# Kernel tuning notes

Hardware: AMD Instinct MI355X
Metric: run time of the kernel (lower is better)

## Reference

```python
import jax, jax.numpy as jnp
import numpy as np

B, DM, DR, DE, E, H, EPS = 4096, 1024, 2048, 1024, 8, 8, 1e-5
SCALE = (DE // H) ** -0.5


def setup_inputs() -> dict:
    key = jax.random.key(0)
    ks = jax.random.split(key, 24)
    n = lambda k, s, sc=0.02: jax.random.normal(k, s, jnp.float32) * sc
    return {
        "x": n(ks[0], (B, DM), 1.0),
        "Wm_mu": n(ks[1], (E, DM, DE)), "bm_mu": jnp.zeros((E, DE)),
        "g_mu": jnp.ones((E, DE)), "be_mu": jnp.zeros((E, DE)),
        "rm_mu": jnp.zeros((E, DE)), "rv_mu": jnp.ones((E, DE)),
        "Wm_d": n(ks[2], (E, DM, DE)), "bm_d": jnp.zeros((E, DE)),
        "g_d": jnp.ones((E, DE)), "be_d": jnp.zeros((E, DE)),
        "rm_d": jnp.zeros((E, DE)), "rv_d": jnp.ones((E, DE)),
        "gw1_mu": n(ks[3], (DM, 64)), "gb1_mu": jnp.zeros((64,)),
        "gw2_mu": n(ks[4], (64, E)), "gb2_mu": jnp.zeros((E,)),
        "gw1_d": n(ks[5], (DM, 64)), "gb1_d": jnp.zeros((64,)),
        "gw2_d": n(ks[6], (64, E)), "gb2_d": jnp.zeros((E,)),
        "Wq": n(ks[7], (DE, DE)), "Wk": n(ks[8], (DE, DE)), "Wv": n(ks[9], (DE, DE)),
        "Wp": n(ks[10], (DE, DE)), "bp": jnp.zeros((DE,)),
        "se_w1": n(ks[11], (DE, DE // 64)), "se_w2": n(ks[12], (DE // 64, DE)),
        "Wr_dec": n(ks[13], (DE, DR)), "br_dec": jnp.zeros((DR,)),
        "gr": jnp.ones((DR,)), "betar": jnp.zeros((DR,)),
        "rmr": jnp.zeros((DR,)), "rvr": jnp.ones((DR,)),
        "Wm_dec": n(ks[14], (DE, DM)), "bm_dec": jnp.zeros((DM,)),
        "gm": jnp.ones((DM,)), "betam": jnp.zeros((DM,)),
        "rmm": jnp.zeros((DM,)), "rvm": jnp.ones((DM,)),
    }


def _bn(h, g, b, rm, rv):  # eval-mode BatchNorm1d
    return (h - rm) * jax.lax.rsqrt(rv + EPS) * g + b


def _moe(x, W, bias, g, be, rm, rv, gw1, gb1, gw2, gb2, act):
    # all-expert Linear+BN+act, gated softmax mixture
    h = jnp.einsum('bd,edh->beh', x, W) + bias            # [B,E,DE]
    h = act(_bn(h, g, be, rm, rv))
    gate = jax.nn.softmax(jax.nn.relu(x @ gw1 + gb1) @ gw2 + gb2, axis=-1)  # [B,E]
    return jnp.einsum('beh,be->bh', h, gate)


def _attn(x, Wq, Wk, Wv, Wp, bp):  # x: [B,N,C], self-attention (context = x)
    b, n, c = x.shape
    hd = c // H
    q = (x @ Wq).reshape(b, n, H, hd).transpose(0, 2, 1, 3)
    k = (x @ Wk).reshape(b, n, H, hd).transpose(0, 2, 1, 3)
    v = (x @ Wv).reshape(b, n, H, hd).transpose(0, 2, 1, 3)
    a = jax.nn.softmax(jnp.einsum('bhnd,bhmd->bhnm', q, k) * SCALE, axis=-1)
    o = jnp.einsum('bhnm,bhmd->bhnd', a, v).transpose(0, 2, 1, 3).reshape(b, n, c)
    return o @ Wp + bp


def reference(x, Wm_mu, bm_mu, g_mu, be_mu, rm_mu, rv_mu,
              Wm_d, bm_d, g_d, be_d, rm_d, rv_d,
              gw1_mu, gb1_mu, gw2_mu, gb2_mu, gw1_d, gb1_d, gw2_d, gb2_d,
              Wq, Wk, Wv, Wp, bp, se_w1, se_w2,
              Wr_dec, br_dec, gr, betar, rmr, rvr,
              Wm_dec, bm_dec, gm, betam, rmm, rvm):
    # Translator.test_model(x, 'MET') == forward_with_MET(x, 'test')
    mu = _moe(x, Wm_mu, bm_mu, g_mu, be_mu, rm_mu, rv_mu,
              gw1_mu, gb1_mu, gw2_mu, gb2_mu, jax.nn.relu)
    d = _moe(x, Wm_d, bm_d, g_d, be_d, rm_d, rv_d,
             gw1_d, gb1_d, gw2_d, gb2_d, jax.nn.relu)
    attn_out = _attn(x[:, None, :], Wq, Wk, Wv, Wp, bp)[:, 0, :]
    mu = mu + attn_out
    latent = mu  # forward_type == 'test'
    # SE layer
    latent = latent * jax.nn.sigmoid(jax.nn.relu(latent @ se_w1) @ se_w2)
    r_out = jax.nn.sigmoid(_bn(latent @ Wr_dec + br_dec, gr, betar, rmr, rvr))
    m_out = jax.nn.sigmoid(_bn(latent @ Wm_dec + bm_dec, gm, betam, rmm, rvm))
    return (r_out, m_out, mu, d)
```

## Files before the change

kernel.cpp:

```cpp
#include <hip/hip_runtime.h>
#include <hip/hip_bf16.h>

typedef __hip_bfloat16 bf16;
typedef __attribute__((ext_vector_type(4))) float f32x4;
typedef __attribute__((ext_vector_type(8))) short s16x8;
typedef __attribute__((ext_vector_type(4))) short s16x4;

#define AS1 __attribute__((address_space(1)))
#define AS3 __attribute__((address_space(3)))

#define NB      4096
#define EPSV    1e-5f

#define OUT_R_OFF   0ull
#define OUT_M_OFF   8388608ull
#define OUT_MU_OFF  12582912ull
#define OUT_D_OFF   16777216ull

__device__ __forceinline__ short f2bf(float f) {
  union { bf16 b; short s; } u;
  u.b = __float2bfloat16(f);
  return u.s;
}
__device__ __forceinline__ float bf2f(short s) {
  union { float f; unsigned u; } v;
  v.u = ((unsigned)(unsigned short)s) << 16;
  return v.f;
}

__device__ __forceinline__ void gl_lds16(const bf16* g, void* l) {
  __builtin_amdgcn_global_load_lds((const AS1 unsigned int*)g,
                                   (AS3 unsigned int*)l, 16, 0, 0);
}

__device__ __forceinline__ void stage_tile_ld1024(const bf16* __restrict__ base,
                                                  int row0, int k0,
                                                  unsigned char* ldsTile,
                                                  int wave, int lane) {
  const int srow = lane >> 3;
  const int gch  = ((lane & 7) + srow) & 7;
  const bf16* g0 = base + ((size_t)(row0 + srow) << 10) + k0 + (gch << 3);
#pragma unroll
  for (int i = 0; i < 4; ++i) {
    const int q = wave * 4 + i;
    gl_lds16(g0 + ((size_t)(q * 8) << 10), ldsTile + (q << 10));
  }
}

__device__ __forceinline__ s16x8 read_frag(const unsigned char* ldsTile, int r, int g) {
  return *(const s16x8*)(ldsTile + r * 128 + (((g - r) & 7) << 4));
}

struct __align__(16) TileLds {
  unsigned char A[16384];
  unsigned char Bm[16384];
  float colScale[128];
  float colShift[128];
  float rowGate[128];
};

__device__ __forceinline__ void mfma_step(const unsigned char* lA, const unsigned char* lB,
                                          int waveM, int waveN, int quad, int l15,
                                          f32x4 acc[4][4]) {
#pragma unroll
  for (int kk = 0; kk < 2; ++kk) {
    const int g = (kk << 2) + quad;
    s16x8 a[4], b[4];
#pragma unroll
    for (int i = 0; i < 4; ++i) a[i] = read_frag(lA, waveM * 64 + i * 16 + l15, g);
#pragma unroll
    for (int j = 0; j < 4; ++j) b[j] = read_frag(lB, waveN * 64 + j * 16 + l15, g);
#pragma unroll
    for (int i = 0; i < 4; ++i)
#pragma unroll
      for (int j = 0; j < 4; ++j)
        acc[i][j] = __builtin_amdgcn_mfma_f32_16x16x32_bf16(a[i], b[j], acc[i][j], 0, 0, 0);
  }
}

__device__ __forceinline__ void tr_tile(const float* __restrict__ src,
                                        short* __restrict__ dst,
                                        int R, int C, int r0, int c0,
                                        short (*t)[68], int tid) {
  const int cc = (tid & 15) * 4;
  const int rr = tid >> 4;
#pragma unroll
  for (int s = 0; s < 4; ++s) {
    const int lr = s * 16 + rr;
    const float4 v = *(const float4*)(src + (size_t)(r0 + lr) * C + c0 + cc);
    s16x4 o;
    o[0] = f2bf(v.x); o[1] = f2bf(v.y); o[2] = f2bf(v.z); o[3] = f2bf(v.w);
    *(s16x4*)(&t[lr][cc]) = o;
  }
  __syncthreads();
#pragma unroll
  for (int s = 0; s < 4; ++s) {
    const int wl = s * 16 + rr;
    s16x4 o;
#pragma unroll
    for (int u = 0; u < 4; ++u) o[u] = t[cc + u][wl];
    *(s16x4*)(dst + (size_t)(c0 + wl) * R + r0 + cc) = o;
  }
}

__global__ __launch_bounds__(256) void prep_tr(
    const float* __restrict__ Wm_mu, const float* __restrict__ Wm_d,
    const float* __restrict__ Wp, const float* __restrict__ gw1_mu,
    const float* __restrict__ gw1_d, const float* __restrict__ se_w1,
    bf16* __restrict__ WmT_mu, bf16* __restrict__ WmT_d,
    bf16* __restrict__ WpT, bf16* __restrict__ Bg, bf16* __restrict__ sw1T) {
  __shared__ short t[64][68];
  const int b = blockIdx.x, tid = threadIdx.x;
  if (b < 2048) {
    const int batch = b >> 8, rem = b & 255;
    const size_t ofs = (size_t)batch << 20;
    tr_tile(Wm_mu + ofs, (short*)WmT_mu + ofs, 1024, 1024,
            (rem >> 4) * 64, (rem & 15) * 64, t, tid);
  } else if (b < 4096) {
    const int bb = b - 2048;
    const int batch = bb >> 8, rem = bb & 255;
    const size_t ofs = (size_t)batch << 20;
    tr_tile(Wm_d + ofs, (short*)WmT_d + ofs, 1024, 1024,
            (rem >> 4) * 64, (rem & 15) * 64, t, tid);
  } else if (b < 4352) {
    const int bb = b - 4096;
    tr_tile(Wp, (short*)WpT, 1024, 1024, (bb >> 4) * 64, (bb & 15) * 64, t, tid);
  } else if (b < 4368) {
    tr_tile(gw1_mu, (short*)Bg, 1024, 64, (b - 4352) * 64, 0, t, tid);
  } else if (b < 4384) {
    tr_tile(gw1_d, (short*)Bg + 65536, 1024, 64, (b - 4368) * 64, 0, t, tid);
  } else {
    const int i = (b - 4384) * 256 + tid;
    const int u = i >> 10, d = i & 1023;
    ((short*)sw1T)[i] = f2bf(se_w1[d * 16 + u]);
  }
}

__global__ __launch_bounds__(256) void prep_cvt(const float* __restrict__ x,
                                                const float* __restrict__ Wv,
                                                const float* __restrict__ se_w2,
                                                bf16* __restrict__ xb,
                                                bf16* __restrict__ Wv_b,
                                                bf16* __restrict__ sw2b) {
  const int i = blockIdx.x * 256 + threadIdx.x;
  const float* src; bf16* dst; int idx;
  if (i < 1048576)      { src = x;     dst = xb;   idx = i; }
  else if (i < 1310720) { src = Wv;    dst = Wv_b; idx = i - 1048576; }
  else if (i < 1311744) { src = se_w2; dst = sw2b; idx = i - 1310720; }
  else return;
  const float4 v = ((const float4*)src)[idx];
  s16x4 o;
  o[0] = f2bf(v.x); o[1] = f2bf(v.y); o[2] = f2bf(v.z); o[3] = f2bf(v.w);
  *(s16x4*)((short*)dst + (size_t)idx * 4) = o;
}

__global__ __launch_bounds__(256) void prep_tr2(const float* __restrict__ Wr_dec,
                                                const float* __restrict__ Wm_dec,
                                                bf16* __restrict__ WrT,
                                                bf16* __restrict__ WmdT) {
  __shared__ short t[64][68];
  const int b = blockIdx.x, tid = threadIdx.x;
  if (b < 512) {
    tr_tile(Wr_dec, (short*)WrT, 1024, 2048, (b >> 5) * 64, (b & 31) * 64, t, tid);
  } else {
    const int bb = b - 512;
    tr_tile(Wm_dec, (short*)WmdT, 1024, 1024, (bb >> 4) * 64, (bb & 15) * 64, t, tid);
  }
}

__global__ __launch_bounds__(256, 2) void gemm_bt(const bf16* __restrict__ A,
                                                  const bf16* __restrict__ Bt,
                                                  bf16* __restrict__ C, int N) {
  __shared__ TileLds lds;
  const int tid = threadIdx.x, lane = tid & 63, wave = tid >> 6;
  const int waveM = wave >> 1, waveN = wave & 1;
  const int quad = lane >> 4, l15 = lane & 15;
  const int m0 = blockIdx.x * 128, n0 = blockIdx.y * 128;
  f32x4 acc[4][4] = {};
  for (int kt = 0; kt < 16; ++kt) {
    __syncthreads();
    stage_tile_ld1024(A, m0, kt << 6, lds.A, wave, lane);
    stage_tile_ld1024(Bt, n0, kt << 6, lds.Bm, wave, lane);
    __builtin_amdgcn_s_waitcnt(0);
    __syncthreads();
    mfma_step(lds.A, lds.Bm, waveM, waveN, quad, l15, acc);
  }
#pragma unroll
  for (int i = 0; i < 4; ++i)
#pragma unroll
    for (int p = 0; p < 4; ++p) {
      const int r = m0 + waveM * 64 + i * 16 + (quad << 2) + p;
#pragma unroll
      for (int j = 0; j < 4; ++j) {
        const int c = n0 + waveN * 64 + j * 16 + l15;
        ((short*)C)[(size_t)r * N + c] = f2bf(acc[i][j][p]);
      }
    }
}

__global__ __launch_bounds__(256) void hgates(const bf16* __restrict__ xb,
                                              const bf16* __restrict__ Bg,
                                              const float* __restrict__ gb1_mu,
                                              const float* __restrict__ gb1_d,
                                              const float* __restrict__ gw2_mu,
                                              const float* __restrict__ gb2_mu,
                                              const float* __restrict__ gw2_d,
                                              const float* __restrict__ gb2_d,
                                              float* __restrict__ gates_mu,
                                              float* __restrict__ gates_d) {
  __shared__ TileLds lds;
  __shared__ float H[128][132];
  __shared__ float w2l[1024];
  __shared__ float b2l[16];
  const int tid = threadIdx.x, lane = tid & 63, wave = tid >> 6;
  const int waveM = wave >> 1, waveN = wave & 1;
  const int quad = lane >> 4, l15 = lane & 15;
  const int m0 = blockIdx.x * 128;
#pragma unroll
  for (int i = 0; i < 4; ++i) {
    const int idx = tid + i * 256;
    w2l[idx] = (idx < 512) ? gw2_mu[idx] : gw2_d[idx - 512];
  }
  if (tid < 16) b2l[tid] = (tid < 8) ? gb2_mu[tid] : gb2_d[tid - 8];
  f32x4 acc[4][4] = {};
  for (int kt = 0; kt < 16; ++kt) {
    __syncthreads();
    stage_tile_ld1024(xb, m0, kt << 6, lds.A, wave, lane);
    stage_tile_ld1024(Bg, 0, kt << 6, lds.Bm, wave, lane);
    __builtin_amdgcn_s_waitcnt(0);
    __syncthreads();
    mfma_step(lds.A, lds.Bm, waveM, waveN, quad, l15, acc);
  }
  float bias[4];
#pragma unroll
  for (int j = 0; j < 4; ++j) {
    const int c = waveN * 64 + j * 16 + l15;
    bias[j] = (c < 64) ? gb1_mu[c] : gb1_d[c - 64];
  }
#pragma unroll
  for (int i = 0; i < 4; ++i)
#pragma unroll
    for (int p = 0; p < 4; ++p) {
      const int r = waveM * 64 + i * 16 + (quad << 2) + p;
#pragma unroll
      for (int j = 0; j < 4; ++j) {
        const int c = waveN * 64 + j * 16 + l15;
        H[r][c] = fmaxf(acc[i][j][p] + bias[j], 0.f);
      }
    }
  __syncthreads();
  const int row = tid >> 1, path = tid & 1;
  float lg[8];
#pragma unroll
  for (int e = 0; e < 8; ++e) lg[e] = b2l[path * 8 + e];
  const float* wp = &w2l[path * 512];
  for (int j = 0; j < 64; ++j) {
    const float hv = H[row][path * 64 + j];
#pragma unroll
    for (int e = 0; e < 8; ++e) lg[e] += hv * wp[j * 8 + e];
  }
  float mx = lg[0];
#pragma unroll
  for (int e = 1; e < 8; ++e) mx = fmaxf(mx, lg[e]);
  float s = 0.f;
#pragma unroll
  for (int e = 0; e < 8; ++e) { lg[e] = __expf(lg[e] - mx); s += lg[e]; }
  const float inv = 1.f / s;
  float* gout = path ? gates_d : gates_mu;
#pragma unroll
  for (int e = 0; e < 8; ++e) gout[((size_t)(m0 + row) << 3) + e] = lg[e] * inv;
}

__global__ __launch_bounds__(256, 2) void moe_fused(
    const bf16* __restrict__ xb, const bf16* __restrict__ WmT_mu, const bf16* __restrict__ WmT_d,
    const bf16* __restrict__ WvpT,
    const float* __restrict__ bm_mu, const float* __restrict__ g_mu, const float* __restrict__ be_mu,
    const float* __restrict__ rm_mu, const float* __restrict__ rv_mu,
    const float* __restrict__ bm_d, const float* __restrict__ g_d, const float* __restrict__ be_d,
    const float* __restrict__ rm_d, const float* __restrict__ rv_d,
    const float* __restrict__ bp,
    const float* __restrict__ gates_mu, const float* __restrict__ gates_d,
    float* __restrict__ out_mu, float* __restrict__ out_d) {
  __shared__ TileLds lds;
  const int tid = threadIdx.x, lane = tid & 63, wave = tid >> 6;
  const int waveM = wave >> 1, waveN = wave & 1;
  const int quad = lane >> 4, l15 = lane & 15;
  const int m0 = blockIdx.x * 128, n0 = blockIdx.y * 128;
  const int path = blockIdx.z;
  const int nExp = (path == 0) ? 9 : 8;
  const bf16* Wall = (path == 0) ? WmT_mu : WmT_d;
  const float* gates = (path == 0) ? gates_mu : gates_d;
  const float* bmP = (path == 0) ? bm_mu : bm_d;
  const float* gP  = (path == 0) ? g_mu : g_d;
  const float* beP = (path == 0) ? be_mu : be_d;
  const float* rmP = (path == 0) ? rm_mu : rm_d;
  const float* rvP = (path == 0) ? rv_mu : rv_d;

  f32x4 fin[4][4] = {};

  for (int e = 0; e < nExp; ++e) {
    const bool isAttn = (path == 0) && (e == 8);
    const bf16* Bmat = isAttn ? WvpT : (Wall + ((size_t)e << 20));
    f32x4 acc[4][4] = {};
    for (int kt = 0; kt < 16; ++kt) {
      __syncthreads();
      stage_tile_ld1024(xb, m0, kt << 6, lds.A, wave, lane);
      stage_tile_ld1024(Bmat, n0, kt << 6, lds.Bm, wave, lane);
      if (kt == 0 && tid < 128) {
        const int c = n0 + tid;
        float sc, sh, gt;
        if (isAttn) {
          sc = 1.f; sh = bp[c]; gt = 1.f;
        } else {
          const int idx = (e << 10) + c;
          sc = gP[idx] * rsqrtf(rvP[idx] + EPSV);
          sh = (bmP[idx] - rmP[idx]) * sc + beP[idx];
          gt = gates[((size_t)(m0 + tid) << 3) + e];
        }
        lds.colScale[tid] = sc;
        lds.colShift[tid] = sh;
        lds.rowGate[tid]  = gt;
      }
      __builtin_amdgcn_s_waitcnt(0);
      __syncthreads();
      mfma_step(lds.A, lds.Bm, waveM, waveN, quad, l15, acc);
    }
#pragma unroll
    for (int i = 0; i < 4; ++i) {
      const int rb = waveM * 64 + i * 16 + (quad << 2);
      float gt[4];
#pragma unroll
      for (int p = 0; p < 4; ++p) gt[p] = lds.rowGate[rb + p];
#pragma unroll
      for (int j = 0; j < 4; ++j) {
        const int c = waveN * 64 + j * 16 + l15;
        const float sc = lds.colScale[c], sh = lds.colShift[c];
#pragma unroll
        for (int p = 0; p < 4; ++p) {
          float v = acc[i][j][p] * sc + sh;
          if (!isAttn) v = fmaxf(v, 0.f);
          fin[i][j][p] += gt[p] * v;
        }
      }
    }
  }
  float* outp = (path == 0) ? out_mu : out_d;
#pragma unroll
  for (int i = 0; i < 4; ++i)
#pragma unroll
    for (int p = 0; p < 4; ++p) {
      const int r = m0 + waveM * 64 + i * 16 + (quad << 2) + p;
#pragma unroll
      for (int j = 0; j < 4; ++j) {
        const int c = n0 + waveN * 64 + j * 16 + l15;
        outp[((size_t)r << 10) + c] = fin[i][j][p];
      }
    }
}

__global__ __launch_bounds__(256) void se3_kernel(const float* __restrict__ mu,
                                                  const bf16* __restrict__ sw1T,
                                                  const bf16* __restrict__ sw2b,
                                                  bf16* __restrict__ latent) {
  __shared__ float part[16][256];
  __shared__ float part2[16][17];
  __shared__ float s1[16];
  const int tid = threadIdx.x;
  for (int r = 0; r < 8; ++r) {
    const int row = blockIdx.x * 8 + r;
    const float4 m = *(const float4*)(mu + ((size_t)row << 10) + tid * 4);
#pragma unroll
    for (int u = 0; u < 16; ++u) {
      const s16x4 w = *(const s16x4*)((const short*)sw1T + u * 1024 + tid * 4);
      part[u][tid] = m.x * bf2f(w[0]) + m.y * bf2f(w[1])
                   + m.z * bf2f(w[2]) + m.w * bf2f(w[3]);
    }
    __syncthreads();
    {
      const int u = tid >> 4, c = tid & 15;
      float s = 0.f;
#pragma unroll
      for (int k = 0; k < 16; ++k) s += part[u][c * 16 + k];
      part2[u][c] = s;
    }
    __syncthreads();
    if (tid < 16) {
      float s = 0.f;
#pragma unroll
      for (int k = 0; k < 16; ++k) s += part2[tid][k];
      s1[tid] = fmaxf(s, 0.f);
    }
    __syncthreads();
    float o[4] = {0.f, 0.f, 0.f, 0.f};
#pragma unroll
    for (int u = 0; u < 16; ++u) {
      const s16x4 w = *(const s16x4*)((const short*)sw2b + u * 1024 + tid * 4);
      const float sv = s1[u];
      o[0] += sv * bf2f(w[0]); o[1] += sv * bf2f(w[1]);
      o[2] += sv * bf2f(w[2]); o[3] += sv * bf2f(w[3]);
    }
    const float mv[4] = {m.x, m.y, m.z, m.w};
    s16x4 ov;
#pragma unroll
    for (int t = 0; t < 4; ++t)
      ov[t] = f2bf(mv[t] / (1.f + __expf(-o[t])));
    *(s16x4*)((short*)latent + ((size_t)row << 10) + tid * 4) = ov;
    __syncthreads();
  }
}

__global__ __launch_bounds__(256, 2) void dec_kernel(
    const bf16* __restrict__ latent, const bf16* __restrict__ WrT, const bf16* __restrict__ WmdT,
    const float* __restrict__ br, const float* __restrict__ gr, const float* __restrict__ betar,
    const float* __restrict__ rmr, const float* __restrict__ rvr,
    const float* __restrict__ bm, const float* __restrict__ gm, const float* __restrict__ betam,
    const float* __restrict__ rmm, const float* __restrict__ rvm,
    float* __restrict__ out) {
  __shared__ TileLds lds;
  const int tid = threadIdx.x, lane = tid & 63, wave = tid >> 6;
  const int waveM = wave >> 1, waveN = wave & 1;
  const int quad = lane >> 4, l15 = lane & 15;
  const int m0 = blockIdx.x * 128;
  const int nt = blockIdx.y;
  const bool isR = nt < 16;
  const int n0 = (isR ? nt : nt - 16) * 128;
  const bf16* Bt = isR ? WrT : WmdT;
  f32x4 acc[4][4] = {};
  for (int kt = 0; kt < 16; ++kt) {
    __syncthreads();
    stage_tile_ld1024(latent, m0, kt << 6, lds.A, wave, lane);
    stage_tile_ld1024(Bt, n0, kt << 6, lds.Bm, wave, lane);
    if (kt == 0 && tid < 128) {
      const int c = n0 + tid;
      const float bb = isR ? br[c] : bm[c];
      const float gg = isR ? gr[c] : gm[c];
      const float be = isR ? betar[c] : betam[c];
      const float rm = isR ? rmr[c] : rmm[c];
      const float rv = isR ? rvr[c] : rvm[c];
      const float sc = gg * rsqrtf(rv + EPSV);
      lds.colScale[tid] = sc;
      lds.colShift[tid] = (bb - rm) * sc + be;
    }
    __builtin_amdgcn_s_waitcnt(0);
    __syncthreads();
    mfma_step(lds.A, lds.Bm, waveM, waveN, quad, l15, acc);
  }
#pragma unroll
  for (int i = 0; i < 4; ++i)
#pragma unroll
    for (int p = 0; p < 4; ++p) {
      const int r = m0 + waveM * 64 + i * 16 + (quad << 2) + p;
#pragma unroll
      for (int j = 0; j < 4; ++j) {
        const int cl = waveN * 64 + j * 16 + l15;
        float v = acc[i][j][p] * lds.colScale[cl] + lds.colShift[cl];
        v = 1.f / (1.f + __expf(-v));
        const size_t idx = isR ? ((size_t)r * 2048 + n0 + cl)
                               : (OUT_M_OFF + (size_t)r * 1024 + n0 + cl);
        out[idx] = v;
      }
    }
}

extern "C" void kernel_launch(void* const* d_in, const int* in_sizes, int n_in,
                              void* d_out, int out_size, void* d_ws, size_t ws_size,
                              hipStream_t stream) {
  (void)in_sizes; (void)n_in; (void)out_size; (void)ws_size;
  const float* x      = (const float*)d_in[0];
  const float* Wm_mu  = (const float*)d_in[1];
  const float* bm_mu  = (const float*)d_in[2];
  const float* g_mu   = (const float*)d_in[3];
  const float* be_mu  = (const float*)d_in[4];
  const float* rm_mu  = (const float*)d_in[5];
  const float* rv_mu  = (const float*)d_in[6];
  const float* Wm_d   = (const float*)d_in[7];
  const float* bm_d   = (const float*)d_in[8];
  const float* g_d    = (const float*)d_in[9];
  const float* be_d   = (const float*)d_in[10];
  const float* rm_d   = (const float*)d_in[11];
  const float* rv_d   = (const float*)d_in[12];
  const float* gw1_mu = (const float*)d_in[13];
  const float* gb1_mu = (const float*)d_in[14];
  const float* gw2_mu = (const float*)d_in[15];
  const float* gb2_mu = (const float*)d_in[16];
  const float* gw1_d  = (const float*)d_in[17];
  const float* gb1_d  = (const float*)d_in[18];
  const float* gw2_d  = (const float*)d_in[19];
  const float* gb2_d  = (const float*)d_in[20];
  const float* Wv     = (const float*)d_in[23];
  const float* Wp     = (const float*)d_in[24];
  const float* bp     = (const float*)d_in[25];
  const float* se_w1  = (const float*)d_in[26];
  const float* se_w2  = (const float*)d_in[27];
  const float* Wr_dec = (const float*)d_in[28];
  const float* br_dec = (const float*)d_in[29];
  const float* gr     = (const float*)d_in[30];
  const float* betar  = (const float*)d_in[31];
  const float* rmr    = (const float*)d_in[32];
  const float* rvr    = (const float*)d_in[33];
  const float* Wm_dec = (const float*)d_in[34];
  const float* bm_dec = (const float*)d_in[35];
  const float* gm     = (const float*)d_in[36];
  const float* betam  = (const float*)d_in[37];
  const float* rmm    = (const float*)d_in[38];
  const float* rvm    = (const float*)d_in[39];

  unsigned char* ws = (unsigned char*)d_ws;
  bf16* xb      = (bf16*)(ws + 0);
  bf16* WmT_mu  = (bf16*)(ws + 8388608);
  bf16* WmT_d   = (bf16*)(ws + 25165824);
  bf16* WvpT    = (bf16*)(ws + 41943040);
  float* gates_mu = (float*)(ws + 44040192);
  float* gates_d  = (float*)(ws + 44171264);
  bf16* latent  = (bf16*)(ws + 0);
  bf16* WrT     = (bf16*)(ws + 8388608);
  bf16* WmdT    = (bf16*)(ws + 12582912);

  float* out = (float*)d_out;
  float* out_mu = out + OUT_MU_OFF;
  float* out_d  = out + OUT_D_OFF;
  bf16* Bg    = (bf16*)(out + 524288);
  bf16* sw1T  = (bf16*)(out + 589824);
  bf16* sw2b  = (bf16*)(out + 598016);
  bf16* WpT   = (bf16*)(out + OUT_MU_OFF);
  bf16* Wv_b  = (bf16*)(out + OUT_MU_OFF + 524288);

  const dim3 blk(256, 1, 1);

  prep_tr<<<dim3(4448, 1, 1), blk, 0, stream>>>(
      Wm_mu, Wm_d, Wp, gw1_mu, gw1_d, se_w1,
      WmT_mu, WmT_d, WpT, Bg, sw1T);
  prep_cvt<<<dim3(5127, 1, 1), blk, 0, stream>>>(x, Wv, se_w2, xb, Wv_b, sw2b);
  gemm_bt<<<dim3(8, 8, 1), blk, 0, stream>>>(WpT, Wv_b, WvpT, 1024);
  hgates<<<dim3(32, 1, 1), blk, 0, stream>>>(xb, Bg, gb1_mu, gb1_d,
                                             gw2_mu, gb2_mu, gw2_d, gb2_d,
                                             gates_mu, gates_d);
  moe_fused<<<dim3(32, 8, 2), blk, 0, stream>>>(
      xb, WmT_mu, WmT_d, WvpT, bm_mu, g_mu, be_mu, rm_mu, rv_mu,
      bm_d, g_d, be_d, rm_d, rv_d, bp, gates_mu, gates_d, out_mu, out_d);
  prep_tr2<<<dim3(768, 1, 1), blk, 0, stream>>>(Wr_dec, Wm_dec, WrT, WmdT);
  se3_kernel<<<dim3(512, 1, 1), blk, 0, stream>>>(out_mu, sw1T, sw2b, latent);
  dec_kernel<<<dim3(32, 24, 1), blk, 0, stream>>>(
      latent, WrT, WmdT, br_dec, gr, betar, rmr, rvr,
      bm_dec, gm, betam, rmm, rvm, out);
}
```

Before: 486.5 us.

## Process expert pairs per pass to reuse A fragments and accumulate outputs in global memory

The MoE kernel now loops over experts two at a time, staging two weight tiles per k-step and reusing the loaded x fragments across both experts' MFMAs. This halves the number of A-tile reloads and barriers per expert. The per-block register accumulator is replaced by read-modify-write accumulation into the output buffer in global memory, and BN scale/shift and gates are read directly from global memory. The cost is a larger LDS footprint (48KB), double accumulator registers that may hurt the 2-blocks-per-CU occupancy, and extra global traffic from repeated output read/write.

```diff
diff --git a/kernel.cpp b/kernel.cpp
--- a/kernel.cpp
+++ b/kernel.cpp
@@ -57,6 +57,11 @@
   float colScale[128];
   float colShift[128];
   float rowGate[128];
+};
+
+struct __align__(16) PairLds {
+  unsigned char A[16384];
+  unsigned char B[2][16384];
 };
 
 __device__ __forceinline__ void mfma_step(const unsigned char* lA, const unsigned char* lB,
@@ -281,7 +286,7 @@
     const float* __restrict__ bp,
     const float* __restrict__ gates_mu, const float* __restrict__ gates_d,
     float* __restrict__ out_mu, float* __restrict__ out_d) {
-  __shared__ TileLds lds;
+  __shared__ PairLds lds;
   const int tid = threadIdx.x, lane = tid & 63, wave = tid >> 6;
   const int waveM = wave >> 1, waveN = wave & 1;
   const int quad = lane >> 4, l15 = lane & 15;
@@ -295,67 +300,91 @@
   const float* beP = (path == 0) ? be_mu : be_d;
   const float* rmP = (path == 0) ? rm_mu : rm_d;
   const float* rvP = (path == 0) ? rv_mu : rv_d;
-
-  f32x4 fin[4][4] = {};
-
-  for (int e = 0; e < nExp; ++e) {
-    const bool isAttn = (path == 0) && (e == 8);
-    const bf16* Bmat = isAttn ? WvpT : (Wall + ((size_t)e << 20));
-    f32x4 acc[4][4] = {};
+  float* outp = (path == 0) ? out_mu : out_d;
+
+  for (int e0 = 0; e0 < nExp; e0 += 2) {
+    const int ne = (nExp - e0 >= 2) ? 2 : 1;
+    const bool attn0 = (path == 0) && (e0 == 8);
+    const bf16* B0 = attn0 ? WvpT : (Wall + ((size_t)e0 << 20));
+    const bf16* B1 = Wall + ((size_t)(e0 + 1) << 20);
+    f32x4 acc[2][4][4] = {};
     for (int kt = 0; kt < 16; ++kt) {
       __syncthreads();
       stage_tile_ld1024(xb, m0, kt << 6, lds.A, wave, lane);
-      stage_tile_ld1024(Bmat, n0, kt << 6, lds.Bm, wave, lane);
-      if (kt == 0 && tid < 128) {
-        const int c = n0 + tid;
-        float sc, sh, gt;
-        if (isAttn) {
-          sc = 1.f; sh = bp[c]; gt = 1.f;
-        } else {
-          const int idx = (e << 10) + c;
-          sc = gP[idx] * rsqrtf(rvP[idx] + EPSV);
-          sh = (bmP[idx] - rmP[idx]) * sc + beP[idx];
-          gt = gates[((size_t)(m0 + tid) << 3) + e];
-        }
-        lds.colScale[tid] = sc;
-        lds.colShift[tid] = sh;
-        lds.rowGate[tid]  = gt;
-      }
+      stage_tile_ld1024(B0, n0, kt << 6, lds.B[0], wave, lane);
+      if (ne == 2) stage_tile_ld1024(B1, n0, kt << 6, lds.B[1], wave, lane);
       __builtin_amdgcn_s_waitcnt(0);
       __syncthreads();
-      mfma_step(lds.A, lds.Bm, waveM, waveN, quad, l15, acc);
-    }
-#pragma unroll
-    for (int i = 0; i < 4; ++i) {
-      const int rb = waveM * 64 + i * 16 + (quad << 2);
-      float gt[4];
-#pragma unroll
-      for (int p = 0; p < 4; ++p) gt[p] = lds.rowGate[rb + p];
-#pragma unroll
-      for (int j = 0; j < 4; ++j) {
-        const int c = waveN * 64 + j * 16 + l15;
-        const float sc = lds.colScale[c], sh = lds.colShift[c];
-#pragma unroll
-        for (int p = 0; p < 4; ++p) {
-          float v = acc[i][j][p] * sc + sh;
-          if (!isAttn) v = fmaxf(v, 0.f);
-          fin[i][j][p] += gt[p] * v;
+#pragma unroll
+      for (int kk = 0; kk < 2; ++kk) {
+        const int g = (kk << 2) + quad;
+        s16x8 a[4], b0[4], b1[4];
+#pragma unroll
+        for (int i = 0; i < 4; ++i) a[i] = read_frag(lds.A, waveM * 64 + i * 16 + l15, g);
+#pragma unroll
+        for (int j = 0; j < 4; ++j) b0[j] = read_frag(lds.B[0], waveN * 64 + j * 16 + l15, g);
+#pragma unroll
+        for (int i = 0; i < 4; ++i)
+#pragma unroll
+          for (int j = 0; j < 4; ++j)
+            acc[0][i][j] = __builtin_amdgcn_mfma_f32_16x16x32_bf16(a[i], b0[j], acc[0][i][j], 0, 0, 0);
+        if (ne == 2) {
+#pragma unroll
+          for (int j = 0; j < 4; ++j) b1[j] = read_frag(lds.B[1], waveN * 64 + j * 16 + l15, g);
+#pragma unroll
+          for (int i = 0; i < 4; ++i)
+#pragma unroll
+            for (int j = 0; j < 4; ++j)
+              acc[1][i][j] = __builtin_amdgcn_mfma_f32_16x16x32_bf16(a[i], b1[j], acc[1][i][j], 0, 0, 0);
         }
       }
     }
-  }
-  float* outp = (path == 0) ? out_mu : out_d;
-#pragma unroll
-  for (int i = 0; i < 4; ++i)
-#pragma unroll
-    for (int p = 0; p < 4; ++p) {
-      const int r = m0 + waveM * 64 + i * 16 + (quad << 2) + p;
+    float sc[2][4], sh[2][4];
+#pragma unroll
+    for (int s = 0; s < 2; ++s) {
+      if (s >= ne) break;
+      const bool isA = (path == 0) && (e0 + s == 8);
 #pragma unroll
       for (int j = 0; j < 4; ++j) {
         const int c = n0 + waveN * 64 + j * 16 + l15;
-        outp[((size_t)r << 10) + c] = fin[i][j][p];
-      }
-    }
+        if (isA) {
+          sc[s][j] = 1.f; sh[s][j] = bp[c];
+        } else {
+          const int idx = ((e0 + s) << 10) + c;
+          const float s_ = gP[idx] * rsqrtf(rvP[idx] + EPSV);
+          sc[s][j] = s_;
+          sh[s][j] = (bmP[idx] - rmP[idx]) * s_ + beP[idx];
+        }
+      }
+    }
+    const bool first = (e0 == 0);
+#pragma unroll
+    for (int i = 0; i < 4; ++i) {
+      const int rb = m0 + waveM * 64 + i * 16 + (quad << 2);
+      float gt0[4], gt1[4];
+#pragma unroll
+      for (int p = 0; p < 4; ++p) {
+        gt0[p] = attn0 ? 1.f : gates[((size_t)(rb + p) << 3) + e0];
+        gt1[p] = (ne == 2) ? gates[((size_t)(rb + p) << 3) + e0 + 1] : 0.f;
+      }
+#pragma unroll
+      for (int j = 0; j < 4; ++j) {
+        const int c = n0 + waveN * 64 + j * 16 + l15;
+#pragma unroll
+        for (int p = 0; p < 4; ++p) {
+          float v0 = acc[0][i][j][p] * sc[0][j] + sh[0][j];
+          if (!attn0) v0 = fmaxf(v0, 0.f);
+          float t = gt0[p] * v0;
+          if (ne == 2) {
+            float v1 = fmaxf(acc[1][i][j][p] * sc[1][j] + sh[1][j], 0.f);
+            t += gt1[p] * v1;
+          }
+          float* po = &outp[((size_t)(rb + p) << 10) + c];
+          *po = (first ? 0.f : *po) + t;
+        }
+      }
+    }
+  }
 }
 
 __global__ __launch_bounds__(256) void se3_kernel(const float* __restrict__ mu,
```

Result: slower. 507.7 us (+4.3%).

## Merge prep, gate and post-MoE launches into fewer combined kernels

Applied to the files above, without the earlier changes.

Several small kernels are merged by blockIdx ranges into single launches: the transpose and convert prep kernels become one, the Wv·Wp GEMM and the gate MLP share a launch, and the decoder weight transposes share a launch with the SE layer. moe_fused now loads BN scale/shift and gate values straight into registers from global memory in its epilogue, instead of staging them in LDS during the first k-step. This cuts kernel launch count and per-launch tail idle time, and shrinks LDS in moe_fused, at the cost of divergent block roles and some extra scattered global loads in the epilogue.

```diff
diff --git a/kernel.cpp b/kernel.cpp
--- a/kernel.cpp
+++ b/kernel.cpp
@@ -51,12 +51,16 @@
   return *(const s16x8*)(ldsTile + r * 128 + (((g - r) & 7) << 4));
 }
 
+struct __align__(16) TileAB {
+  unsigned char A[16384];
+  unsigned char Bm[16384];
+};
+
 struct __align__(16) TileLds {
   unsigned char A[16384];
   unsigned char Bm[16384];
   float colScale[128];
   float colShift[128];
-  float rowGate[128];
 };
 
 __device__ __forceinline__ void mfma_step(const unsigned char* lA, const unsigned char* lB,
@@ -103,12 +107,15 @@
   }
 }
 
-__global__ __launch_bounds__(256) void prep_tr(
+__global__ __launch_bounds__(256) void prep_all(
     const float* __restrict__ Wm_mu, const float* __restrict__ Wm_d,
     const float* __restrict__ Wp, const float* __restrict__ gw1_mu,
     const float* __restrict__ gw1_d, const float* __restrict__ se_w1,
+    const float* __restrict__ x, const float* __restrict__ Wv,
+    const float* __restrict__ se_w2,
     bf16* __restrict__ WmT_mu, bf16* __restrict__ WmT_d,
-    bf16* __restrict__ WpT, bf16* __restrict__ Bg, bf16* __restrict__ sw1T) {
+    bf16* __restrict__ WpT, bf16* __restrict__ Bg, bf16* __restrict__ sw1T,
+    bf16* __restrict__ xb, bf16* __restrict__ Wv_b, bf16* __restrict__ sw2b) {
   __shared__ short t[64][68];
   const int b = blockIdx.x, tid = threadIdx.x;
   if (b < 2048) {
@@ -129,146 +136,117 @@
     tr_tile(gw1_mu, (short*)Bg, 1024, 64, (b - 4352) * 64, 0, t, tid);
   } else if (b < 4384) {
     tr_tile(gw1_d, (short*)Bg + 65536, 1024, 64, (b - 4368) * 64, 0, t, tid);
-  } else {
+  } else if (b < 4448) {
     const int i = (b - 4384) * 256 + tid;
     const int u = i >> 10, d = i & 1023;
     ((short*)sw1T)[i] = f2bf(se_w1[d * 16 + u]);
-  }
-}
-
-__global__ __launch_bounds__(256) void prep_cvt(const float* __restrict__ x,
-                                                const float* __restrict__ Wv,
-                                                const float* __restrict__ se_w2,
-                                                bf16* __restrict__ xb,
-                                                bf16* __restrict__ Wv_b,
-                                                bf16* __restrict__ sw2b) {
-  const int i = blockIdx.x * 256 + threadIdx.x;
-  const float* src; bf16* dst; int idx;
-  if (i < 1048576)      { src = x;     dst = xb;   idx = i; }
-  else if (i < 1310720) { src = Wv;    dst = Wv_b; idx = i - 1048576; }
-  else if (i < 1311744) { src = se_w2; dst = sw2b; idx = i - 1310720; }
-  else return;
-  const float4 v = ((const float4*)src)[idx];
-  s16x4 o;
-  o[0] = f2bf(v.x); o[1] = f2bf(v.y); o[2] = f2bf(v.z); o[3] = f2bf(v.w);
-  *(s16x4*)((short*)dst + (size_t)idx * 4) = o;
-}
-
-__global__ __launch_bounds__(256) void prep_tr2(const float* __restrict__ Wr_dec,
-                                                const float* __restrict__ Wm_dec,
-                                                bf16* __restrict__ WrT,
-                                                bf16* __restrict__ WmdT) {
-  __shared__ short t[64][68];
-  const int b = blockIdx.x, tid = threadIdx.x;
-  if (b < 512) {
-    tr_tile(Wr_dec, (short*)WrT, 1024, 2048, (b >> 5) * 64, (b & 31) * 64, t, tid);
   } else {
-    const int bb = b - 512;
-    tr_tile(Wm_dec, (short*)WmdT, 1024, 1024, (bb >> 4) * 64, (bb & 15) * 64, t, tid);
-  }
-}
-
-__global__ __launch_bounds__(256, 2) void gemm_bt(const bf16* __restrict__ A,
-                                                  const bf16* __restrict__ Bt,
-                                                  bf16* __restrict__ C, int N) {
-  __shared__ TileLds lds;
-  const int tid = threadIdx.x, lane = tid & 63, wave = tid >> 6;
-  const int waveM = wave >> 1, waveN = wave & 1;
-  const int quad = lane >> 4, l15 = lane & 15;
-  const int m0 = blockIdx.x * 128, n0 = blockIdx.y * 128;
-  f32x4 acc[4][4] = {};
-  for (int kt = 0; kt < 16; ++kt) {
-    __syncthreads();
-    stage_tile_ld1024(A, m0, kt << 6, lds.A, wave, lane);
-    stage_tile_ld1024(Bt, n0, kt << 6, lds.Bm, wave, lane);
-    __builtin_amdgcn_s_waitcnt(0);
-    __syncthreads();
-    mfma_step(lds.A, lds.Bm, waveM, waveN, quad, l15, acc);
-  }
-#pragma unroll
-  for (int i = 0; i < 4; ++i)
-#pragma unroll
-    for (int p = 0; p < 4; ++p) {
-      const int r = m0 + waveM * 64 + i * 16 + (quad << 2) + p;
-#pragma unroll
-      for (int j = 0; j < 4; ++j) {
-        const int c = n0 + waveN * 64 + j * 16 + l15;
-        ((short*)C)[(size_t)r * N + c] = f2bf(acc[i][j][p]);
-      }
-    }
-}
-
-__global__ __launch_bounds__(256) void hgates(const bf16* __restrict__ xb,
-                                              const bf16* __restrict__ Bg,
-                                              const float* __restrict__ gb1_mu,
-                                              const float* __restrict__ gb1_d,
-                                              const float* __restrict__ gw2_mu,
-                                              const float* __restrict__ gb2_mu,
-                                              const float* __restrict__ gw2_d,
-                                              const float* __restrict__ gb2_d,
-                                              float* __restrict__ gates_mu,
-                                              float* __restrict__ gates_d) {
-  __shared__ TileLds lds;
+    const int i = (b - 4448) * 256 + tid;
+    const float* src; bf16* dst; int idx;
+    if (i < 1048576)      { src = x;     dst = xb;   idx = i; }
+    else if (i < 1310720) { src = Wv;    dst = Wv_b; idx = i - 1048576; }
+    else if (i < 1311744) { src = se_w2; dst = sw2b; idx = i - 1310720; }
+    else return;
+    const float4 v = ((const float4*)src)[idx];
+    s16x4 o;
+    o[0] = f2bf(v.x); o[1] = f2bf(v.y); o[2] = f2bf(v.z); o[3] = f2bf(v.w);
+    *(s16x4*)((short*)dst + (size_t)idx * 4) = o;
+  }
+}
+
+__global__ __launch_bounds__(256) void gemm_gate(
+    const bf16* __restrict__ WpT, const bf16* __restrict__ Wv_b,
+    bf16* __restrict__ WvpT,
+    const bf16* __restrict__ xb, const bf16* __restrict__ Bg,
+    const float* __restrict__ gb1_mu, const float* __restrict__ gb1_d,
+    const float* __restrict__ gw2_mu, const float* __restrict__ gb2_mu,
+    const float* __restrict__ gw2_d, const float* __restrict__ gb2_d,
+    float* __restrict__ gates_mu, float* __restrict__ gates_d) {
+  __shared__ TileAB lds;
   __shared__ float H[128][132];
   __shared__ float w2l[1024];
   __shared__ float b2l[16];
   const int tid = threadIdx.x, lane = tid & 63, wave = tid >> 6;
   const int waveM = wave >> 1, waveN = wave & 1;
   const int quad = lane >> 4, l15 = lane & 15;
-  const int m0 = blockIdx.x * 128;
-#pragma unroll
-  for (int i = 0; i < 4; ++i) {
-    const int idx = tid + i * 256;
-    w2l[idx] = (idx < 512) ? gw2_mu[idx] : gw2_d[idx - 512];
-  }
-  if (tid < 16) b2l[tid] = (tid < 8) ? gb2_mu[tid] : gb2_d[tid - 8];
-  f32x4 acc[4][4] = {};
-  for (int kt = 0; kt < 16; ++kt) {
+  if (blockIdx.x < 64) {
+    const int m0 = (blockIdx.x & 7) * 128, n0 = (blockIdx.x >> 3) * 128;
+    f32x4 acc[4][4] = {};
+    for (int kt = 0; kt < 16; ++kt) {
+      __syncthreads();
+      stage_tile_ld1024(WpT, m0, kt << 6, lds.A, wave, lane);
+      stage_tile_ld1024(Wv_b, n0, kt << 6, lds.Bm, wave, lane);
+      __builtin_amdgcn_s_waitcnt(0);
+      __syncthreads();
+      mfma_step(lds.A, lds.Bm, waveM, waveN, quad, l15, acc);
+    }
+#pragma unroll
+    for (int i = 0; i < 4; ++i)
+#pragma unroll
+      for (int p = 0; p < 4; ++p) {
+        const int r = m0 + waveM * 64 + i * 16 + (quad << 2) + p;
+#pragma unroll
+        for (int j = 0; j < 4; ++j) {
+          const int c = n0 + waveN * 64 + j * 16 + l15;
+          ((short*)WvpT)[(size_t)r * 1024 + c] = f2bf(acc[i][j][p]);
+        }
+      }
+  } else {
+    const int m0 = (blockIdx.x - 64) * 128;
+#pragma unroll
+    for (int i = 0; i < 4; ++i) {
+      const int idx = tid + i * 256;
+      w2l[idx] = (idx < 512) ? gw2_mu[idx] : gw2_d[idx - 512];
+    }
+    if (tid < 16) b2l[tid] = (tid < 8) ? gb2_mu[tid] : gb2_d[tid - 8];
+    f32x4 acc[4][4] = {};
+    for (int kt = 0; kt < 16; ++kt) {
+      __syncthreads();
+      stage_tile_ld1024(xb, m0, kt << 6, lds.A, wave, lane);
+      stage_tile_ld1024(Bg, 0, kt << 6, lds.Bm, wave, lane);
+      __builtin_amdgcn_s_waitcnt(0);
+      __syncthreads();
+      mfma_step(lds.A, lds.Bm, waveM, waveN, quad, l15, acc);
+    }
+    float bias[4];
+#pragma unroll
+    for (int j = 0; j < 4; ++j) {
+      const int c = waveN * 64 + j * 16 + l15;
+      bias[j] = (c < 64) ? gb1_mu[c] : gb1_d[c - 64];
+    }
+#pragma unroll
+    for (int i = 0; i < 4; ++i)
+#pragma unroll
+      for (int p = 0; p < 4; ++p) {
+        const int r = waveM * 64 + i * 16 + (quad << 2) + p;
+#pragma unroll
+        for (int j = 0; j < 4; ++j) {
+          const int c = waveN * 64 + j * 16 + l15;
+          H[r][c] = fmaxf(acc[i][j][p] + bias[j], 0.f);
+        }
+      }
     __syncthreads();
-    stage_tile_ld1024(xb, m0, kt << 6, lds.A, wave, lane);
-    stage_tile_ld1024(Bg, 0, kt << 6, lds.Bm, wave, lane);
-    __builtin_amdgcn_s_waitcnt(0);
-    __syncthreads();
-    mfma_step(lds.A, lds.Bm, waveM, waveN, quad, l15, acc);
-  }
-  float bias[4];
-#pragma unroll
-  for (int j = 0; j < 4; ++j) {
-    const int c = waveN * 64 + j * 16 + l15;
-    bias[j] = (c < 64) ? gb1_mu[c] : gb1_d[c - 64];
-  }
-#pragma unroll
-  for (int i = 0; i < 4; ++i)
-#pragma unroll
-    for (int p = 0; p < 4; ++p) {
-      const int r = waveM * 64 + i * 16 + (quad << 2) + p;
-#pragma unroll
-      for (int j = 0; j < 4; ++j) {
-        const int c = waveN * 64 + j * 16 + l15;
-        H[r][c] = fmaxf(acc[i][j][p] + bias[j], 0.f);
-      }
-    }
-  __syncthreads();
-  const int row = tid >> 1, path = tid & 1;
-  float lg[8];
-#pragma unroll
-  for (int e = 0; e < 8; ++e) lg[e] = b2l[path * 8 + e];
-  const float* wp = &w2l[path * 512];
-  for (int j = 0; j < 64; ++j) {
-    const float hv = H[row][path * 64 + j];
-#pragma unroll
-    for (int e = 0; e < 8; ++e) lg[e] += hv * wp[j * 8 + e];
-  }
-  float mx = lg[0];
-#pragma unroll
-  for (int e = 1; e < 8; ++e) mx = fmaxf(mx, lg[e]);
-  float s = 0.f;
-#pragma unroll
-  for (int e = 0; e < 8; ++e) { lg[e] = __expf(lg[e] - mx); s += lg[e]; }
-  const float inv = 1.f / s;
-  float* gout = path ? gates_d : gates_mu;
-#pragma unroll
-  for (int e = 0; e < 8; ++e) gout[((size_t)(m0 + row) << 3) + e] = lg[e] * inv;
+    const int row = tid >> 1, path = tid & 1;
+    float lg[8];
+#pragma unroll
+    for (int e = 0; e < 8; ++e) lg[e] = b2l[path * 8 + e];
+    const float* wp = &w2l[path * 512];
+    for (int j = 0; j < 64; ++j) {
+      const float hv = H[row][path * 64 + j];
+#pragma unroll
+      for (int e = 0; e < 8; ++e) lg[e] += hv * wp[j * 8 + e];
+    }
+    float mx = lg[0];
+#pragma unroll
+    for (int e = 1; e < 8; ++e) mx = fmaxf(mx, lg[e]);
+    float s = 0.f;
+#pragma unroll
+    for (int e = 0; e < 8; ++e) { lg[e] = __expf(lg[e] - mx); s += lg[e]; }
+    const float inv = 1.f / s;
+    float* gout = path ? gates_d : gates_mu;
+#pragma unroll
+    for (int e = 0; e < 8; ++e) gout[((size_t)(m0 + row) << 3) + e] = lg[e] * inv;
+  }
 }
 
 __global__ __launch_bounds__(256, 2) void moe_fused(
@@ -281,7 +259,7 @@
     const float* __restrict__ bp,
     const float* __restrict__ gates_mu, const float* __restrict__ gates_d,
     float* __restrict__ out_mu, float* __restrict__ out_d) {
-  __shared__ TileLds lds;
+  __shared__ TileAB lds;
   const int tid = threadIdx.x, lane = tid & 63, wave = tid >> 6;
   const int waveM = wave >> 1, waveN = wave & 1;
   const int quad = lane >> 4, l15 = lane & 15;
@@ -306,42 +284,38 @@
       __syncthreads();
       stage_tile_ld1024(xb, m0, kt << 6, lds.A, wave, lane);
       stage_tile_ld1024(Bmat, n0, kt << 6, lds.Bm, wave, lane);
-      if (kt == 0 && tid < 128) {
-        const int c = n0 + tid;
-        float sc, sh, gt;
-        if (isAttn) {
-          sc = 1.f; sh = bp[c]; gt = 1.f;
-        } else {
-          const int idx = (e << 10) + c;
-          sc = gP[idx] * rsqrtf(rvP[idx] + EPSV);
-          sh = (bmP[idx] - rmP[idx]) * sc + beP[idx];
-          gt = gates[((size_t)(m0 + tid) << 3) + e];
-        }
-        lds.colScale[tid] = sc;
-        lds.colShift[tid] = sh;
-        lds.rowGate[tid]  = gt;
-      }
       __builtin_amdgcn_s_waitcnt(0);
       __syncthreads();
       mfma_step(lds.A, lds.Bm, waveM, waveN, quad, l15, acc);
     }
+    float sc[4], sh[4];
+#pragma unroll
+    for (int j = 0; j < 4; ++j) {
+      const int c = n0 + waveN * 64 + j * 16 + l15;
+      if (isAttn) {
+        sc[j] = 1.f; sh[j] = bp[c];
+      } else {
+        const int idx = (e << 10) + c;
+        const float s_ = gP[idx] * rsqrtf(rvP[idx] + EPSV);
+        sc[j] = s_;
+        sh[j] = (bmP[idx] - rmP[idx]) * s_ + beP[idx];
+      }
+    }
 #pragma unroll
     for (int i = 0; i < 4; ++i) {
-      const int rb = waveM * 64 + i * 16 + (quad << 2);
+      const int rb = m0 + waveM * 64 + i * 16 + (quad << 2);
       float gt[4];
 #pragma unroll
-      for (int p = 0; p < 4; ++p) gt[p] = lds.rowGate[rb + p];
-#pragma unroll
-      for (int j = 0; j < 4; ++j) {
-        const int c = waveN * 64 + j * 16 + l15;
-        const float sc = lds.colScale[c], sh = lds.colShift[c];
+      for (int p = 0; p < 4; ++p)
+        gt[p] = isAttn ? 1.f : gates[((size_t)(rb + p) << 3) + e];
+#pragma unroll
+      for (int j = 0; j < 4; ++j)
 #pragma unroll
         for (int p = 0; p < 4; ++p) {
-          float v = acc[i][j][p] * sc + sh;
+          float v = acc[i][j][p] * sc[j] + sh[j];
           if (!isAttn) v = fmaxf(v, 0.f);
           fin[i][j][p] += gt[p] * v;
         }
-      }
     }
   }
   float* outp = (path == 0) ? out_mu : out_d;
@@ -358,54 +332,64 @@
     }
 }
 
-__global__ __launch_bounds__(256) void se3_kernel(const float* __restrict__ mu,
-                                                  const bf16* __restrict__ sw1T,
-                                                  const bf16* __restrict__ sw2b,
-                                                  bf16* __restrict__ latent) {
+__global__ __launch_bounds__(256) void post_moe(
+    const float* __restrict__ Wr_dec, const float* __restrict__ Wm_dec,
+    bf16* __restrict__ WrT, bf16* __restrict__ WmdT,
+    const float* __restrict__ mu, const bf16* __restrict__ sw1T,
+    const bf16* __restrict__ sw2b, bf16* __restrict__ latent) {
+  __shared__ short t[64][68];
   __shared__ float part[16][256];
   __shared__ float part2[16][17];
   __shared__ float s1[16];
-  const int tid = threadIdx.x;
-  for (int r = 0; r < 8; ++r) {
-    const int row = blockIdx.x * 8 + r;
-    const float4 m = *(const float4*)(mu + ((size_t)row << 10) + tid * 4);
-#pragma unroll
-    for (int u = 0; u < 16; ++u) {
-      const s16x4 w = *(const s16x4*)((const short*)sw1T + u * 1024 + tid * 4);
-      part[u][tid] = m.x * bf2f(w[0]) + m.y * bf2f(w[1])
-                   + m.z * bf2f(w[2]) + m.w * bf2f(w[3]);
-    }
-    __syncthreads();
-    {
-      const int u = tid >> 4, c = tid & 15;
-      float s = 0.f;
-#pragma unroll
-      for (int k = 0; k < 16; ++k) s += part[u][c * 16 + k];
-      part2[u][c] = s;
-    }
-    __syncthreads();
-    if (tid < 16) {
-      float s = 0.f;
-#pragma unroll
-      for (int k = 0; k < 16; ++k) s += part2[tid][k];
-      s1[tid] = fmaxf(s, 0.f);
-    }
-    __syncthreads();
-    float o[4] = {0.f, 0.f, 0.f, 0.f};
-#pragma unroll
-    for (int u = 0; u < 16; ++u) {
-      const s16x4 w = *(const s16x4*)((const short*)sw2b + u * 1024 + tid * 4);
-      const float sv = s1[u];
-      o[0] += sv * bf2f(w[0]); o[1] += sv * bf2f(w[1]);
-      o[2] += sv * bf2f(w[2]); o[3] += sv * bf2f(w[3]);
-    }
-    const float mv[4] = {m.x, m.y, m.z, m.w};
-    s16x4 ov;
-#pragma unroll
-    for (int t = 0; t < 4; ++t)
-      ov[t] = f2bf(mv[t] / (1.f + __expf(-o[t])));
-    *(s16x4*)((short*)latent + ((size_t)row << 10) + tid * 4) = ov;
-    __syncthreads();
+  const int b = blockIdx.x, tid = threadIdx.x;
+  if (b < 512) {
+    tr_tile(Wr_dec, (short*)WrT, 1024, 2048, (b >> 5) * 64, (b & 31) * 64, t, tid);
+  } else if (b < 768) {
+    const int bb = b - 512;
+    tr_tile(Wm_dec, (short*)WmdT, 1024, 1024, (bb >> 4) * 64, (bb & 15) * 64, t, tid);
+  } else {
+    const int blk = b - 768;
+    for (int r = 0; r < 8; ++r) {
+      const int row = blk * 8 + r;
+      const float4 m = *(const float4*)(mu + ((size_t)row << 10) + tid * 4);
+#pragma unroll
+      for (int u = 0; u < 16; ++u) {
+        const s16x4 w = *(const s16x4*)((const short*)sw1T + u * 1024 + tid * 4);
+        part[u][tid] = m.x * bf2f(w[0]) + m.y * bf2f(w[1])
+                     + m.z * bf2f(w[2]) + m.w * bf2f(w[3]);
+      }
+      __syncthreads();
+      {
+        const int u = tid >> 4, c = tid & 15;
+        float s = 0.f;
+#pragma unroll
+        for (int k = 0; k < 16; ++k) s += part[u][c * 16 + k];
+        part2[u][c] = s;
+      }
+      __syncthreads();
+      if (tid < 16) {
+        float s = 0.f;
+#pragma unroll
+        for (int k = 0; k < 16; ++k) s += part2[tid][k];
+        s1[tid] = fmaxf(s, 0.f);
+      }
+      __syncthreads();
+      float o[4] = {0.f, 0.f, 0.f, 0.f};
+#pragma unroll
+      for (int u = 0; u < 16; ++u) {
+        const s16x4 w = *(const s16x4*)((const short*)sw2b + u * 1024 + tid * 4);
+        const float sv = s1[u];
+        o[0] += sv * bf2f(w[0]); o[1] += sv * bf2f(w[1]);
+        o[2] += sv * bf2f(w[2]); o[3] += sv * bf2f(w[3]);
+      }
+      const float mv[4] = {m.x, m.y, m.z, m.w};
+      s16x4 ov;
+#pragma unroll
+      for (int tt = 0; tt < 4; ++tt)
+        ov[tt] = f2bf(mv[tt] / (1.f + __expf(-o[tt])));
+      *(s16x4*)((short*)latent + ((size_t)row << 10) + tid * 4) = ov;
+      __syncthreads();
+    }
   }
 }
 
@@ -527,19 +511,17 @@
 
   const dim3 blk(256, 1, 1);
 
-  prep_tr<<<dim3(4448, 1, 1), blk, 0, stream>>>(
-      Wm_mu, Wm_d, Wp, gw1_mu, gw1_d, se_w1,
-      WmT_mu, WmT_d, WpT, Bg, sw1T);
-  prep_cvt<<<dim3(5127, 1, 1), blk, 0, stream>>>(x, Wv, se_w2, xb, Wv_b, sw2b);
-  gemm_bt<<<dim3(8, 8, 1), blk, 0, stream>>>(WpT, Wv_b, WvpT, 1024);
-  hgates<<<dim3(32, 1, 1), blk, 0, stream>>>(xb, Bg, gb1_mu, gb1_d,
-                                             gw2_mu, gb2_mu, gw2_d, gb2_d,
-                                             gates_mu, gates_d);
+  prep_all<<<dim3(9575, 1, 1), blk, 0, stream>>>(
+      Wm_mu, Wm_d, Wp, gw1_mu, gw1_d, se_w1, x, Wv, se_w2,
+      WmT_mu, WmT_d, WpT, Bg, sw1T, xb, Wv_b, sw2b);
+  gemm_gate<<<dim3(96, 1, 1), blk, 0, stream>>>(
+      WpT, Wv_b, WvpT, xb, Bg, gb1_mu, gb1_d,
+      gw2_mu, gb2_mu, gw2_d, gb2_d, gates_mu, gates_d);
   moe_fused<<<dim3(32, 8, 2), blk, 0, stream>>>(
       xb, WmT_mu, WmT_d, WvpT, bm_mu, g_mu, be_mu, rm_mu, rv_mu,
       bm_d, g_d, be_d, rm_d, rv_d, bp, gates_mu, gates_d, out_mu, out_d);
-  prep_tr2<<<dim3(768, 1, 1), blk, 0, stream>>>(Wr_dec, Wm_dec, WrT, WmdT);
-  se3_kernel<<<dim3(512, 1, 1), blk, 0, stream>>>(out_mu, sw1T, sw2b, latent);
+  post_moe<<<dim3(1280, 1, 1), blk, 0, stream>>>(
+      Wr_dec, Wm_dec, WrT, WmdT, out_mu, sw1T, sw2b, latent);
   dec_kernel<<<dim3(32, 24, 1), blk, 0, stream>>>(
       latent, WrT, WmdT, br_dec, gr, betar, rmr, rvr,
       bm_dec, gm, betam, rmm, rvm, out);
```

After: 465.2 us. 1.05x faster.
